# Optimization experiments

Measured on AMD Instinct MI355X. Metric: run time of the kernel, lower is better.

Reference implementation:

```python
import jax, jax.numpy as jnp
import numpy as np
import math

B = 262144
STATE = 6
TOTAL_MEAS = 27
HID = 256
INPUT_DIM = TOTAL_MEAS * 2 + 1 + STATE + 12  # 73
PI = math.pi
NORM_R_SCALE = 500.0 / 150000.0
ANG_IDX = np.array([0, 1, 3, 4, 6, 9, 10, 12, 13, 15, 18, 19, 21, 22, 24])
ANG_MASK = np.zeros((TOTAL_MEAS,), dtype=bool)
ANG_MASK[ANG_IDX] = True


def setup_inputs() -> dict:
    key = jax.random.key(0)
    ks = jax.random.split(key, 16)
    s = lambda fan: 1.0 / math.sqrt(fan)
    inp = {
        "meas": jax.random.normal(ks[0], (B, TOTAL_MEAS), jnp.float32),
        "mask": jnp.ones((B, TOTAL_MEAS), jnp.float32),
        "dt": jax.random.uniform(ks[1], (B,), jnp.float32),
        "baselines": jax.random.normal(ks[2], (B, 12), jnp.float32),
        "x_prev": jax.random.normal(ks[3], (B, STATE), jnp.float32),
        "hx": jnp.zeros((B, HID), jnp.float32),
        # GRU params (torch gate order: r, z, n)
        "W_ih": jax.random.uniform(ks[4], (3 * HID, INPUT_DIM), jnp.float32, -s(HID), s(HID)),
        "W_hh": jax.random.uniform(ks[5], (3 * HID, HID), jnp.float32, -s(HID), s(HID)),
        "b_ih": jax.random.uniform(ks[6], (3 * HID,), jnp.float32, -s(HID), s(HID)),
        "b_hh": jax.random.uniform(ks[7], (3 * HID,), jnp.float32, -s(HID), s(HID)),
        # LayerNorm
        "ln_g": jnp.ones((HID,), jnp.float32),
        "ln_b": jnp.zeros((HID,), jnp.float32),
        # MLP head: 256 -> 256 -> 128 -> 6*27
        "W1": jax.random.uniform(ks[8], (256, HID), jnp.float32, -s(HID), s(HID)),
        "b1": jax.random.uniform(ks[9], (256,), jnp.float32, -s(HID), s(HID)),
        "W2": jax.random.uniform(ks[10], (128, 256), jnp.float32, -s(256), s(256)),
        "b2": jax.random.uniform(ks[11], (128,), jnp.float32, -s(256), s(256)),
        "W3": jax.random.uniform(ks[12], (STATE * TOTAL_MEAS, 128), jnp.float32, -s(128), s(128)),
        "b3": jax.random.uniform(ks[13], (STATE * TOTAL_MEAS,), jnp.float32, -s(128), s(128)),
    }
    return inp


def _wrap_angle(a):
    two_pi = 2.0 * PI
    return a - two_pi * jnp.round(a / two_pi)


def _platform_y_pred(x_rel):
    # x_rel: [B, 6] -> [B, 9] radar/EO measurement
    r_xy = jnp.sqrt(x_rel[:, 0] ** 2 + x_rel[:, 2] ** 2 + 1e-9)
    az = jnp.arctan2(x_rel[:, 2], x_rel[:, 0]) / PI
    el = jnp.arctan2(x_rel[:, 4], r_xy) / PI
    r = jnp.sqrt(x_rel[:, 0] ** 2 + x_rel[:, 2] ** 2 + x_rel[:, 4] ** 2 + 1e-9)
    z = jnp.zeros_like(r)
    return jnp.stack([az, el, r, az, el, z, az, z, z], axis=1)


def _forward(meas, mask, dt, baselines, x_prev, hx,
             W_ih, W_hh, b_ih, b_hh, ln_g, ln_b, W1, b1, W2, b2, W3, b3):
    # f_predict (CV model): x0 += dt*x1, x2 += dt*x3, x4 += dt*x5
    dt_scaled = dt * NORM_R_SCALE  # [B]
    zcol = jnp.zeros_like(x_prev[:, :1])
    shift = jnp.concatenate([x_prev[:, 1:2], zcol, x_prev[:, 3:4], zcol, x_prev[:, 5:6], zcol], axis=1)
    x_minus = x_prev + dt_scaled[:, None] * shift  # [B, 6]

    y_pred = jnp.concatenate([
        _platform_y_pred(x_minus),
        _platform_y_pred(x_minus - baselines[:, 0:6]),
        _platform_y_pred(x_minus - baselines[:, 6:12]),
    ], axis=1)  # [B, 27]

    innov = meas - y_pred
    wrapped = _wrap_angle(innov * PI) / PI
    innov = jnp.where(jnp.asarray(ANG_MASK)[None, :], wrapped, innov)
    innov = innov * mask

    rnn_in = jnp.concatenate([innov, mask, dt[:, None], x_minus, baselines], axis=1)  # [B, 73]

    # single-step GRU (torch semantics, gate order r,z,n)
    gi = rnn_in @ W_ih.T + b_ih  # [B, 3H]
    gh = hx @ W_hh.T + b_hh      # [B, 3H]
    gi_r, gi_z, gi_n = jnp.split(gi, 3, axis=1)
    gh_r, gh_z, gh_n = jnp.split(gh, 3, axis=1)
    r = jax.nn.sigmoid(gi_r + gh_r)
    z = jax.nn.sigmoid(gi_z + gh_z)
    n = jnp.tanh(gi_n + r * gh_n)
    h_new = (1.0 - z) * n + z * hx  # [B, H]

    # LayerNorm
    mu = jnp.mean(h_new, axis=-1, keepdims=True)
    var = jnp.var(h_new, axis=-1, keepdims=True)
    h_ln = (h_new - mu) / jnp.sqrt(var + 1e-5) * ln_g + ln_b

    # MLP gain head (dropout inactive at inference)
    f1 = jax.nn.relu(h_ln @ W1.T + b1)
    f2 = jax.nn.relu(f1 @ W2.T + b2)
    K = (f2 @ W3.T + b3).reshape(-1, STATE, TOTAL_MEAS)
    K = jnp.clip(K, -3.0, 3.0)

    correction = jnp.einsum('bsm,bm->bs', K, innov)
    x_new = jnp.clip(x_minus + correction, -5.0, 5.0)
    return x_new, h_new


def reference(meas, mask, dt, baselines, x_prev, hx,
              W_ih, W_hh, b_ih, b_hh, ln_g, ln_b, W1, b1, W2, b2, W3, b3):
    return _forward(meas, mask, dt, baselines, x_prev, hx,
                    W_ih, W_hh, b_ih, b_hh, ln_g, ln_b, W1, b1, W2, b2, W3, b3)
```

## Files before the change

### kernel.cpp

```cpp
#include <hip/hip_runtime.h>
#include <math.h>

#define B_TOTAL  262144
#define ROWS     128
#define NWG      (B_TOTAL/ROWS)
#define NTHR     512
#define PI_F     3.14159265358979323846f
#define NORM_R   (500.0f/150000.0f)

typedef float  f32x4  __attribute__((ext_vector_type(4)));
typedef short  bf16x8 __attribute__((ext_vector_type(8)));

#define W_TOTAL (49*8192)

#define LDS_RB   0
#define LDS_HB   34816
#define LDS_STG  100352
#define LDS_XMC  149504
#define LDS_LNS  152576
#define LDS_TOTAL 156672

#define WAIT_VM2 asm volatile("s_waitcnt vmcnt(2)" ::: "memory")
#define WAIT_VM0 asm volatile("s_waitcnt vmcnt(0)" ::: "memory")
#define BARv     __builtin_amdgcn_s_barrier()

__device__ __forceinline__ ushort f2bf(float f){
    union { float f; unsigned u; } v; v.f = f;
    unsigned r = v.u + 0x7FFFu + ((v.u >> 16) & 1u);
    return (ushort)(r >> 16);
}
__device__ __forceinline__ float b2f(ushort u){
    union { unsigned u; float f; } v; v.u = ((unsigned)u) << 16;
    return v.f;
}
__device__ __forceinline__ unsigned pk2(float a, float b){
    return (unsigned)f2bf(a) | ((unsigned)f2bf(b) << 16);
}
__device__ __forceinline__ float upk(unsigned u, int hi){
    return b2f((ushort)(hi ? (u >> 16) : (u & 0xffffu)));
}
__device__ __forceinline__ float sigm(float x){ return 1.0f/(1.0f+__expf(-x)); }
__device__ __forceinline__ float tanh_(float x){ return 1.0f - 2.0f/(__expf(2.0f*x)+1.0f); }
__device__ __forceinline__ int swzb(int row, int k){
    return ((row<<9) + (k<<1)) ^ ((row&7)<<4);
}
__device__ __forceinline__ bf16x8 rdW(const char* gb, int col, int lk){
    int slot = lk ^ ((col >> 1) & 3);
    return *(const bf16x8*)(gb + col*64 + slot*16);
}
__device__ __forceinline__ void stage16(const ushort* src, char* dst, int w, int lane){
    #pragma unroll
    for (int i = 0; i < 2; ++i)
        __builtin_amdgcn_global_load_lds(
            (const __attribute__((address_space(1))) void*)(src + (size_t)((w*2+i)*64 + lane)*8),
            (__attribute__((address_space(3))) void*)(dst + (w*2+i)*1024),
            16, 0, 0);
}
#define PH(g) do { \
    if ((g) == 48) WAIT_VM0; else WAIT_VM2; \
    BARv; \
    if ((g)+2 <= 48) stage16(ws + (size_t)((g)+2)*8192, STG + (((g)+2)%3)*16384, w, lane); \
} while(0)

__device__ __forceinline__ void ldA4_rb(const ushort* Rbu, int mh, int lr, int kb, int lk8, bf16x8 a[4]){
    #pragma unroll
    for (int i = 0; i < 4; ++i)
        a[i] = *(const bf16x8*)(Rbu + (mh*64 + i*16 + lr)*104 + kb*32 + lk8);
}
__device__ __forceinline__ void ldA4_hb(const char* Hb, int mh, int lr, int kb, int lk8, bf16x8 a[4]){
    #pragma unroll
    for (int i = 0; i < 4; ++i)
        a[i] = *(const bf16x8*)(Hb + swzb(mh*64 + i*16 + lr, kb*32 + lk8));
}
__device__ __forceinline__ void mmW(const char* base, int colbase, int lr, int lk,
                                    const bf16x8 a[4], f32x4 acc[4][4]){
    #pragma unroll
    for (int j = 0; j < 4; ++j) {
        bf16x8 wf = rdW(base, colbase + j*16 + lr, lk);
        #pragma unroll
        for (int i = 0; i < 4; ++i)
            acc[i][j] = __builtin_amdgcn_mfma_f32_16x16x32_bf16(wf, a[i], acc[i][j], 0,0,0);
    }
}

__global__ void prep_weights(const float* __restrict__ W_ih, const float* __restrict__ W_hh,
                             const float* __restrict__ W1, const float* __restrict__ W2,
                             const float* __restrict__ W3, ushort* __restrict__ ws)
{
    int id = blockIdx.x*256 + threadIdx.x;
    if (id >= W_TOTAL) return;
    int g = id >> 13;
    int u = id & 8191;
    float v = 0.0f;
    if (g >= 41 && g < 45) {
        int half = u >> 12, u2 = u & 4095;
        int col = u2 >> 5, v5 = u2 & 31, slot = v5 >> 3, e = v5 & 7;
        int kq = slot ^ ((col >> 1) & 3);
        int kb = (g-41)*2 + half;
        v = W2[col*256 + kb*32 + kq*8 + e];
    } else {
        int col = u >> 5, v5 = u & 31, slot = v5 >> 3, e = v5 & 7;
        int kq = slot ^ ((col >> 1) & 3);
        if (g < 3) {
            int k = g*32 + kq*8 + e;
            if (k < 73) v = W_ih[(512+col)*73 + k];
        } else if (g < 11) {
            int k = (g-3)*32 + kq*8 + e;
            v = W_hh[(512+col)*256 + k];
        } else if (g < 22) {
            int k = (g-11)*32 + kq*8 + e;
            v = (k < 73) ? W_ih[col*73 + k] : ((k < 96) ? 0.0f : W_hh[col*256 + (k-96)]);
        } else if (g < 33) {
            int k = (g-22)*32 + kq*8 + e;
            v = (k < 73) ? W_ih[(256+col)*73 + k] : ((k < 96) ? 0.0f : W_hh[(256+col)*256 + (k-96)]);
        } else if (g < 41) {
            int k = (g-33)*32 + kq*8 + e;
            v = W1[col*256 + k];
        } else {
            int k = (g-45)*32 + kq*8 + e;
            if (col < 162) v = W3[col*128 + k];
        }
    }
    ws[id] = f2bf(v);
}

__global__ __launch_bounds__(NTHR, 1) void knet_mfma(
    const float* __restrict__ meas, const float* __restrict__ mask,
    const float* __restrict__ dt,   const float* __restrict__ baselines,
    const float* __restrict__ x_prev, const float* __restrict__ hx,
    const float* __restrict__ b_ih, const float* __restrict__ b_hh,
    const float* __restrict__ ln_g, const float* __restrict__ ln_b,
    const float* __restrict__ b1,   const float* __restrict__ b2,
    const float* __restrict__ b3,
    const ushort* __restrict__ ws,
    float* __restrict__ out)
{
    extern __shared__ char smem[];
    ushort* Rbu  = (ushort*)(smem + LDS_RB);
    char*   Hb   = smem + LDS_HB;
    char*   STG  = smem + LDS_STG;
    float*  xmc  = (float*)(smem + LDS_XMC);
    float*  lnscr= (float*)(smem + LDS_LNS);

    const int tid  = threadIdx.x;
    const int w    = __builtin_amdgcn_readfirstlane(tid >> 6);
    const int nq   = w & 3;
    const int mh   = w >> 2;
    const int lane = tid & 63;
    const int lr   = lane & 15;
    const int lk   = lane >> 4;
    const int lk8  = lk * 8;
    const int row0 = blockIdx.x * ROWS;
    float* hout = out + (size_t)B_TOTAL*6;

    stage16(ws,          STG,          w, lane);
    stage16(ws + 8192,   STG + 16384,  w, lane);

    float* scr = (float*)Hb;
    {
        const size_t m0 = (size_t)row0*27;
        for (int i = tid; i < 3456; i += NTHR) scr[i]        = meas[m0 + i];
        for (int i = tid; i < 3456; i += NTHR) scr[3456 + i] = mask[m0 + i];
        for (int i = tid; i < 1536; i += NTHR) scr[6912 + i] = baselines[(size_t)row0*12 + i];
        for (int i = tid; i < 768;  i += NTHR) scr[8448 + i] = x_prev[(size_t)row0*6 + i];
        if (tid < 128) scr[9216 + tid] = dt[row0 + tid];
    }
    __syncthreads();

    {
        const int part = w >> 1;
        const int row  = (w & 1)*64 + lane;
        const float dtv = scr[9216 + row];
        const float dts = dtv * NORM_R;
        float xp[6], xm[6];
        #pragma unroll
        for (int s = 0; s < 6; ++s) xp[s] = scr[8448 + row*6 + s];
        xm[0] = xp[0] + dts*xp[1]; xm[1] = xp[1];
        xm[2] = xp[2] + dts*xp[3]; xm[3] = xp[3];
        xm[4] = xp[4] + dts*xp[5]; xm[5] = xp[5];
        if (part < 3) {
            float xr[6];
            #pragma unroll
            for (int s = 0; s < 6; ++s) {
                float b = (part == 0) ? 0.0f : scr[6912 + row*12 + (part-1)*6 + s];
                xr[s] = xm[s] - b;
            }
            float rxy = sqrtf(xr[0]*xr[0] + xr[2]*xr[2] + 1e-9f);
            float azv = atan2f(xr[2], xr[0]) * (1.0f/PI_F);
            float elv = atan2f(xr[4], rxy)   * (1.0f/PI_F);
            float rrv = sqrtf(xr[0]*xr[0] + xr[2]*xr[2] + xr[4]*xr[4] + 1e-9f);
            float y[9] = {azv, elv, rrv, azv, elv, 0.0f, azv, 0.0f, 0.0f};
            const bool ang[9] = {true,true,false,true,true,false,true,false,false};
            #pragma unroll
            for (int i = 0; i < 9; ++i) {
                int m = part*9 + i;
                float ms = scr[3456 + row*27 + m];
                float v  = scr[row*27 + m] - y[i];
                if (ang[i]) v = v - 2.0f*rintf(v*0.5f);
                v *= ms;
                Rbu[row*104 + m]      = f2bf(v);
                Rbu[row*104 + 27 + m] = f2bf(ms);
            }
        } else {
            Rbu[row*104 + 54] = f2bf(dtv);
            #pragma unroll
            for (int s = 0; s < 6; ++s) Rbu[row*104 + 55 + s] = f2bf(xm[s]);
            #pragma unroll
            for (int q = 0; q < 12; ++q) Rbu[row*104 + 61 + q] = f2bf(scr[6912 + row*12 + q]);
            #pragma unroll
            for (int k = 73; k < 96; ++k) Rbu[row*104 + k] = 0;
            #pragma unroll
            for (int s = 0; s < 6; ++s) xmc[row*6 + s] = xm[s];
        }
    }
    __syncthreads();

    {
        const size_t hbase = (size_t)row0 * 256;
        #pragma unroll
        for (int ii = 0; ii < 8; ++ii) {
            int cid = tid + ii*NTHR;
            int r  = cid >> 5;
            int k0 = (cid & 31) << 3;
            const float4* p = (const float4*)(hx + hbase + (size_t)r*256 + k0);
            float4 u = p[0], v2 = p[1];
            bf16x8 o;
            o[0]=(short)f2bf(u.x);  o[1]=(short)f2bf(u.y);  o[2]=(short)f2bf(u.z);  o[3]=(short)f2bf(u.w);
            o[4]=(short)f2bf(v2.x); o[5]=(short)f2bf(v2.y); o[6]=(short)f2bf(v2.z); o[7]=(short)f2bf(v2.w);
            *(bf16x8*)(Hb + swzb(r, k0)) = o;
        }
    }
    __syncthreads();

    unsigned ginp[4][4][2], ghnp[4][4][2];

    {
        f32x4 acc[4][4];
        #pragma unroll
        for (int i = 0; i < 4; ++i)
            #pragma unroll
            for (int j = 0; j < 4; ++j) acc[i][j] = (f32x4){0,0,0,0};
        #pragma unroll
        for (int p = 0; p < 3; ++p) {
            PH(p);
            bf16x8 a[4];
            ldA4_rb(Rbu, mh, lr, p, lk8, a);
            __builtin_amdgcn_s_setprio(1);
            mmW(STG + (p%3)*16384, nq*64, lr, lk, a, acc);
            __builtin_amdgcn_s_setprio(0);
        }
        #pragma unroll
        for (int j = 0; j < 4; ++j) {
            const int c0 = nq*64 + j*16 + lk*4;
            f32x4 b4 = *(const f32x4*)(b_ih + 512 + c0);
            #pragma unroll
            for (int i = 0; i < 4; ++i) {
                ginp[i][j][0] = pk2(acc[i][j][0] + b4[0], acc[i][j][1] + b4[1]);
                ginp[i][j][1] = pk2(acc[i][j][2] + b4[2], acc[i][j][3] + b4[3]);
            }
        }
    }
    {
        f32x4 acc[4][4];
        #pragma unroll
        for (int i = 0; i < 4; ++i)
            #pragma unroll
            for (int j = 0; j < 4; ++j) acc[i][j] = (f32x4){0,0,0,0};
        #pragma unroll
        for (int p = 0; p < 8; ++p) {
            PH(3+p);
            bf16x8 a[4];
            ldA4_hb(Hb, mh, lr, p, lk8, a);
            __builtin_amdgcn_s_setprio(1);
            mmW(STG + ((3+p)%3)*16384, nq*64, lr, lk, a, acc);
            __builtin_amdgcn_s_setprio(0);
        }
        #pragma unroll
        for (int j = 0; j < 4; ++j) {
            const int c0 = nq*64 + j*16 + lk*4;
            f32x4 b4 = *(const f32x4*)(b_hh + 512 + c0);
            #pragma unroll
            for (int i = 0; i < 4; ++i) {
                ghnp[i][j][0] = pk2(acc[i][j][0] + b4[0], acc[i][j][1] + b4[1]);
                ghnp[i][j][1] = pk2(acc[i][j][2] + b4[2], acc[i][j][3] + b4[3]);
            }
        }
    }
    unsigned npk[4][4][2];
    {
        f32x4 acc[4][4];
        #pragma unroll
        for (int i = 0; i < 4; ++i)
            #pragma unroll
            for (int j = 0; j < 4; ++j) acc[i][j] = (f32x4){0,0,0,0};
        #pragma unroll
        for (int p = 0; p < 11; ++p) {
            PH(11+p);
            bf16x8 a[4];
            if (p < 3) ldA4_rb(Rbu, mh, lr, p, lk8, a);
            else       ldA4_hb(Hb, mh, lr, p-3, lk8, a);
            __builtin_amdgcn_s_setprio(1);
            mmW(STG + ((11+p)%3)*16384, nq*64, lr, lk, a, acc);
            __builtin_amdgcn_s_setprio(0);
        }
        #pragma unroll
        for (int j = 0; j < 4; ++j) {
            const int c0 = nq*64 + j*16 + lk*4;
            f32x4 bi4 = *(const f32x4*)(b_ih + c0);
            f32x4 bh4 = *(const f32x4*)(b_hh + c0);
            #pragma unroll
            for (int i = 0; i < 4; ++i) {
                float nv[4];
                #pragma unroll
                for (int e = 0; e < 4; ++e) {
                    float rg = sigm(acc[i][j][e] + bi4[e] + bh4[e]);
                    float gin = upk(ginp[i][j][e>>1], e&1);
                    float ghn = upk(ghnp[i][j][e>>1], e&1);
                    nv[e] = tanh_(gin + rg*ghn);
                }
                npk[i][j][0] = pk2(nv[0], nv[1]);
                npk[i][j][1] = pk2(nv[2], nv[3]);
            }
        }
    }
    float lsum[4] = {0,0,0,0}, lsq[4] = {0,0,0,0};
    {
        f32x4 acc[4][4];
        #pragma unroll
        for (int i = 0; i < 4; ++i)
            #pragma unroll
            for (int j = 0; j < 4; ++j) acc[i][j] = (f32x4){0,0,0,0};
        #pragma unroll
        for (int p = 0; p < 11; ++p) {
            PH(22+p);
            bf16x8 a[4];
            if (p < 3) ldA4_rb(Rbu, mh, lr, p, lk8, a);
            else       ldA4_hb(Hb, mh, lr, p-3, lk8, a);
            __builtin_amdgcn_s_setprio(1);
            mmW(STG + ((22+p)%3)*16384, nq*64, lr, lk, a, acc);
            __builtin_amdgcn_s_setprio(0);
        }
        #pragma unroll
        for (int j = 0; j < 4; ++j) {
            const int c0 = nq*64 + j*16 + lk*4;
            f32x4 bi4 = *(const f32x4*)(b_ih + 256 + c0);
            f32x4 bh4 = *(const f32x4*)(b_hh + 256 + c0);
            #pragma unroll
            for (int i = 0; i < 4; ++i) {
                const int row = mh*64 + i*16 + lr;
                uint2 hxd = *(const uint2*)(Hb + swzb(row, c0));
                float hn4[4];
                #pragma unroll
                for (int e = 0; e < 4; ++e) {
                    float zg = sigm(acc[i][j][e] + bi4[e] + bh4[e]);
                    float nv = upk(npk[i][j][e>>1], e&1);
                    float hxv = upk(e < 2 ? hxd.x : hxd.y, e&1);
                    float hn = (1.0f - zg)*nv + zg*hxv;
                    hn4[e] = hn; lsum[i] += hn; lsq[i] += hn*hn;
                }
                uint2 o;
                o.x = pk2(hn4[0], hn4[1]);
                o.y = pk2(hn4[2], hn4[3]);
                *(uint2*)(Hb + swzb(row, c0)) = o;
                float4 st = { hn4[0], hn4[1], hn4[2], hn4[3] };
                *(float4*)(hout + (size_t)(row0+row)*256 + c0) = st;
            }
        }
    }
    #pragma unroll
    for (int i = 0; i < 4; ++i) {
        lsum[i] += __shfl_xor(lsum[i], 16); lsum[i] += __shfl_xor(lsum[i], 32);
        lsq[i]  += __shfl_xor(lsq[i], 16);  lsq[i]  += __shfl_xor(lsq[i], 32);
    }
    if (lk == 0) {
        #pragma unroll
        for (int i = 0; i < 4; ++i) {
            const int row = mh*64 + i*16 + lr;
            lnscr[row*8 + nq*2 + 0] = lsum[i];
            lnscr[row*8 + nq*2 + 1] = lsq[i];
        }
    }
    __syncthreads();

    {
        float mu[4], rstd[4];
        #pragma unroll
        for (int i = 0; i < 4; ++i) {
            const int row = mh*64 + i*16 + lr;
            float s = 0, q = 0;
            #pragma unroll
            for (int qq = 0; qq < 4; ++qq) { s += lnscr[row*8 + qq*2]; q += lnscr[row*8 + qq*2 + 1]; }
            mu[i] = s * (1.0f/256.0f);
            rstd[i] = rsqrtf(q*(1.0f/256.0f) - mu[i]*mu[i] + 1e-5f);
        }
        #pragma unroll
        for (int j = 0; j < 4; ++j) {
            const int c0 = nq*64 + j*16 + lk*4;
            f32x4 g4 = *(const f32x4*)(ln_g + c0);
            f32x4 b4 = *(const f32x4*)(ln_b + c0);
            #pragma unroll
            for (int i = 0; i < 4; ++i) {
                const int row = mh*64 + i*16 + lr;
                uint2 d = *(const uint2*)(Hb + swzb(row, c0));
                float v0 = (upk(d.x,0)-mu[i])*rstd[i]*g4[0] + b4[0];
                float v1 = (upk(d.x,1)-mu[i])*rstd[i]*g4[1] + b4[1];
                float v2 = (upk(d.y,0)-mu[i])*rstd[i]*g4[2] + b4[2];
                float v3 = (upk(d.y,1)-mu[i])*rstd[i]*g4[3] + b4[3];
                uint2 o; o.x = pk2(v0, v1); o.y = pk2(v2, v3);
                *(uint2*)(Hb + swzb(row, c0)) = o;
            }
        }
    }
    __syncthreads();

    {
        f32x4 acc[4][4];
        #pragma unroll
        for (int i = 0; i < 4; ++i)
            #pragma unroll
            for (int j = 0; j < 4; ++j) acc[i][j] = (f32x4){0,0,0,0};
        #pragma unroll
        for (int p = 0; p < 8; ++p) {
            PH(33+p);
            bf16x8 a[4];
            ldA4_hb(Hb, mh, lr, p, lk8, a);
            __builtin_amdgcn_s_setprio(1);
            mmW(STG + ((33+p)%3)*16384, nq*64, lr, lk, a, acc);
            __builtin_amdgcn_s_setprio(0);
        }
        __syncthreads();
        #pragma unroll
        for (int j = 0; j < 4; ++j) {
            const int c0 = nq*64 + j*16 + lk*4;
            f32x4 b4 = *(const f32x4*)(b1 + c0);
            #pragma unroll
            for (int i = 0; i < 4; ++i) {
                const int row = mh*64 + i*16 + lr;
                uint2 o;
                o.x = pk2(fmaxf(acc[i][j][0]+b4[0],0.f), fmaxf(acc[i][j][1]+b4[1],0.f));
                o.y = pk2(fmaxf(acc[i][j][2]+b4[2],0.f), fmaxf(acc[i][j][3]+b4[3],0.f));
                *(uint2*)(Hb + swzb(row, c0)) = o;
            }
        }
    }
    __syncthreads();

    f32x4 c3[4][2];
    #pragma unroll
    for (int i = 0; i < 4; ++i)
        #pragma unroll
        for (int j = 0; j < 2; ++j) c3[i][j] = (f32x4){0,0,0,0};
    #pragma unroll
    for (int p = 0; p < 4; ++p) {
        PH(41+p);
        const char* sb = STG + ((41+p)%3)*16384;
        #pragma unroll
        for (int h = 0; h < 2; ++h) {
            bf16x8 a[4];
            ldA4_hb(Hb, mh, lr, 2*p + h, lk8, a);
            __builtin_amdgcn_s_setprio(1);
            #pragma unroll
            for (int j = 0; j < 2; ++j) {
                bf16x8 wf = rdW(sb + h*8192, nq*32 + j*16 + lr, lk);
                #pragma unroll
                for (int i = 0; i < 4; ++i)
                    c3[i][j] = __builtin_amdgcn_mfma_f32_16x16x32_bf16(wf, a[i], c3[i][j], 0,0,0);
            }
            __builtin_amdgcn_s_setprio(0);
        }
    }
    f32x4 iv[4][3];
    #pragma unroll
    for (int j = 0; j < 3; ++j)
        #pragma unroll
        for (int i = 0; i < 4; ++i) {
            const int row = mh*64 + i*16 + lr;
            #pragma unroll
            for (int e = 0; e < 4; ++e) {
                int col = nq*48 + j*16 + lk*4 + e;
                int m = col - 27*(col/27);
                iv[i][j][e] = b2f(Rbu[row*104 + m]);
            }
        }
    __syncthreads();
    #pragma unroll
    for (int j = 0; j < 2; ++j) {
        const int c0 = nq*32 + j*16 + lk*4;
        f32x4 b4 = *(const f32x4*)(b2 + c0);
        #pragma unroll
        for (int i = 0; i < 4; ++i) {
            const int row = mh*64 + i*16 + lr;
            uint2 o;
            o.x = pk2(fmaxf(c3[i][j][0]+b4[0],0.f), fmaxf(c3[i][j][1]+b4[1],0.f));
            o.y = pk2(fmaxf(c3[i][j][2]+b4[2],0.f), fmaxf(c3[i][j][3]+b4[3],0.f));
            *(uint2*)((char*)Rbu + row*272 + c0*2) = o;
        }
    }
    __syncthreads();

    {
        f32x4 c4[4][3];
        #pragma unroll
        for (int i = 0; i < 4; ++i)
            #pragma unroll
            for (int j = 0; j < 3; ++j) c4[i][j] = (f32x4){0,0,0,0};
        #pragma unroll
        for (int p = 0; p < 4; ++p) {
            PH(45+p);
            const char* sb = STG + ((45+p)%3)*16384;
            bf16x8 a[4];
            #pragma unroll
            for (int i = 0; i < 4; ++i)
                a[i] = *(const bf16x8*)((const char*)Rbu + (mh*64 + i*16 + lr)*272 + (p*32 + lk8)*2);
            __builtin_amdgcn_s_setprio(1);
            #pragma unroll
            for (int j = 0; j < 3; ++j) {
                bf16x8 wf = rdW(sb, nq*48 + j*16 + lr, lk);
                #pragma unroll
                for (int i = 0; i < 4; ++i)
                    c4[i][j] = __builtin_amdgcn_mfma_f32_16x16x32_bf16(wf, a[i], c4[i][j], 0,0,0);
            }
            __builtin_amdgcn_s_setprio(0);
        }
        #pragma unroll
        for (int j = 0; j < 3; ++j)
            #pragma unroll
            for (int i = 0; i < 4; ++i) {
                const int row = mh*64 + i*16 + lr;
                #pragma unroll
                for (int e = 0; e < 4; ++e) {
                    int col = nq*48 + j*16 + lk*4 + e;
                    if (col < 162) {
                        int s = col / 27;
                        float K = fminf(fmaxf(c4[i][j][e] + b3[col], -3.0f), 3.0f);
                        atomicAdd(&xmc[row*6 + s], K * iv[i][j][e]);
                    }
                }
            }
    }
    __syncthreads();

    for (int t = tid; t < ROWS*6; t += NTHR) {
        int row = t / 6, s = t - row*6;
        float v = fminf(fmaxf(xmc[t], -5.0f), 5.0f);
        out[(size_t)(row0+row)*6 + s] = v;
    }
}

extern "C" void kernel_launch(void* const* d_in, const int* in_sizes, int n_in,
                              void* d_out, int out_size, void* d_ws, size_t ws_size,
                              hipStream_t stream) {
    const float* meas      = (const float*)d_in[0];
    const float* mask      = (const float*)d_in[1];
    const float* dtv       = (const float*)d_in[2];
    const float* baselines = (const float*)d_in[3];
    const float* x_prev    = (const float*)d_in[4];
    const float* hx        = (const float*)d_in[5];
    const float* W_ih      = (const float*)d_in[6];
    const float* W_hh      = (const float*)d_in[7];
    const float* b_ih      = (const float*)d_in[8];
    const float* b_hh      = (const float*)d_in[9];
    const float* ln_g      = (const float*)d_in[10];
    const float* ln_b      = (const float*)d_in[11];
    const float* W1        = (const float*)d_in[12];
    const float* b1        = (const float*)d_in[13];
    const float* W2        = (const float*)d_in[14];
    const float* b2        = (const float*)d_in[15];
    const float* W3        = (const float*)d_in[16];
    const float* b3        = (const float*)d_in[17];
    ushort* wsb = (ushort*)d_ws;
    float* outp = (float*)d_out;

    prep_weights<<<(W_TOTAL + 255)/256, 256, 0, stream>>>(W_ih, W_hh, W1, W2, W3, wsb);
    knet_mfma<<<NWG, NTHR, LDS_TOTAL, stream>>>(
        meas, mask, dtv, baselines, x_prev, hx,
        b_ih, b_hh, ln_g, ln_b, b1, b2, b3, wsb, outp);
}
```

Before: 773.1 us.

## Halve rows per workgroup to run two 256-thread workgroups per CU

Cuts each workgroup to 64 rows and 4 waves and shrinks LDS to about 80KB so two workgroups can share a CU (launch_bounds 2). The weight staging ring drops from triple to double buffering, and a barrier is added after each MMA phase to protect the buffer being reloaded. LayerNorm is rewritten so each row is reduced by 4 threads, removing the cross-wave scratch. Innovation values are reread from LDS at the final step instead of being held in registers. The intent is better latency hiding through occupancy, at the cost of more barriers, twice as many weight reloads per row, and shallower prefetch.

```diff
diff --git a/kernel.cpp b/kernel.cpp
--- a/kernel.cpp
+++ b/kernel.cpp
@@ -2,9 +2,9 @@
 #include <math.h>
 
 #define B_TOTAL  262144
-#define ROWS     128
+#define ROWS     64
 #define NWG      (B_TOTAL/ROWS)
-#define NTHR     512
+#define NTHR     256
 #define PI_F     3.14159265358979323846f
 #define NORM_R   (500.0f/150000.0f)
 
@@ -14,15 +14,15 @@
 #define W_TOTAL (49*8192)
 
 #define LDS_RB   0
-#define LDS_HB   34816
-#define LDS_STG  100352
-#define LDS_XMC  149504
-#define LDS_LNS  152576
-#define LDS_TOTAL 156672
-
-#define WAIT_VM2 asm volatile("s_waitcnt vmcnt(2)" ::: "memory")
-#define WAIT_VM0 asm volatile("s_waitcnt vmcnt(0)" ::: "memory")
-#define BARv     __builtin_amdgcn_s_barrier()
+#define LDS_HB   13312
+#define LDS_STG  46080
+#define LDS_XMC  78848
+#define LDS_TOTAL 80384
+
+#define WAIT_VM4  asm volatile("s_waitcnt vmcnt(4)" ::: "memory")
+#define WAIT_VM0  asm volatile("s_waitcnt vmcnt(0)" ::: "memory")
+#define WAIT_LGKM asm volatile("s_waitcnt lgkmcnt(0)" ::: "memory")
+#define BARv      __builtin_amdgcn_s_barrier()
 
 __device__ __forceinline__ ushort f2bf(float f){
     union { float f; unsigned u; } v; v.f = f;
@@ -50,27 +50,27 @@
 }
 __device__ __forceinline__ void stage16(const ushort* src, char* dst, int w, int lane){
     #pragma unroll
-    for (int i = 0; i < 2; ++i)
+    for (int i = 0; i < 4; ++i)
         __builtin_amdgcn_global_load_lds(
-            (const __attribute__((address_space(1))) void*)(src + (size_t)((w*2+i)*64 + lane)*8),
-            (__attribute__((address_space(3))) void*)(dst + (w*2+i)*1024),
+            (const __attribute__((address_space(1))) void*)(src + (size_t)((w*4+i)*64 + lane)*8),
+            (__attribute__((address_space(3))) void*)(dst + (w*4+i)*1024),
             16, 0, 0);
 }
 #define PH(g) do { \
-    if ((g) == 48) WAIT_VM0; else WAIT_VM2; \
+    if ((g) < 48) stage16(ws + (size_t)((g)+1)*8192, STG + (((g)+1)&1)*16384, w, lane); \
+    if ((g) < 48) WAIT_VM4; else WAIT_VM0; \
     BARv; \
-    if ((g)+2 <= 48) stage16(ws + (size_t)((g)+2)*8192, STG + (((g)+2)%3)*16384, w, lane); \
 } while(0)
 
-__device__ __forceinline__ void ldA4_rb(const ushort* Rbu, int mh, int lr, int kb, int lk8, bf16x8 a[4]){
+__device__ __forceinline__ void ldA4_rb(const ushort* Rbu, int lr, int kb, int lk8, bf16x8 a[4]){
     #pragma unroll
     for (int i = 0; i < 4; ++i)
-        a[i] = *(const bf16x8*)(Rbu + (mh*64 + i*16 + lr)*104 + kb*32 + lk8);
-}
-__device__ __forceinline__ void ldA4_hb(const char* Hb, int mh, int lr, int kb, int lk8, bf16x8 a[4]){
+        a[i] = *(const bf16x8*)(Rbu + (i*16 + lr)*104 + kb*32 + lk8);
+}
+__device__ __forceinline__ void ldA4_hb(const char* Hb, int lr, int kb, int lk8, bf16x8 a[4]){
     #pragma unroll
     for (int i = 0; i < 4; ++i)
-        a[i] = *(const bf16x8*)(Hb + swzb(mh*64 + i*16 + lr, kb*32 + lk8));
+        a[i] = *(const bf16x8*)(Hb + swzb(i*16 + lr, kb*32 + lk8));
 }
 __device__ __forceinline__ void mmW(const char* base, int colbase, int lr, int lk,
                                     const bf16x8 a[4], f32x4 acc[4][4]){
@@ -124,7 +124,7 @@
     ws[id] = f2bf(v);
 }
 
-__global__ __launch_bounds__(NTHR, 1) void knet_mfma(
+__global__ __launch_bounds__(NTHR, 2) void knet_mfma(
     const float* __restrict__ meas, const float* __restrict__ mask,
     const float* __restrict__ dt,   const float* __restrict__ baselines,
     const float* __restrict__ x_prev, const float* __restrict__ hx,
@@ -140,12 +140,10 @@
     char*   Hb   = smem + LDS_HB;
     char*   STG  = smem + LDS_STG;
     float*  xmc  = (float*)(smem + LDS_XMC);
-    float*  lnscr= (float*)(smem + LDS_LNS);
 
     const int tid  = threadIdx.x;
     const int w    = __builtin_amdgcn_readfirstlane(tid >> 6);
-    const int nq   = w & 3;
-    const int mh   = w >> 2;
+    const int nq   = w;
     const int lane = tid & 63;
     const int lr   = lane & 15;
     const int lk   = lane >> 4;
@@ -153,36 +151,34 @@
     const int row0 = blockIdx.x * ROWS;
     float* hout = out + (size_t)B_TOTAL*6;
 
-    stage16(ws,          STG,          w, lane);
-    stage16(ws + 8192,   STG + 16384,  w, lane);
+    stage16(ws, STG, w, lane);
 
     float* scr = (float*)Hb;
     {
         const size_t m0 = (size_t)row0*27;
-        for (int i = tid; i < 3456; i += NTHR) scr[i]        = meas[m0 + i];
-        for (int i = tid; i < 3456; i += NTHR) scr[3456 + i] = mask[m0 + i];
-        for (int i = tid; i < 1536; i += NTHR) scr[6912 + i] = baselines[(size_t)row0*12 + i];
-        for (int i = tid; i < 768;  i += NTHR) scr[8448 + i] = x_prev[(size_t)row0*6 + i];
-        if (tid < 128) scr[9216 + tid] = dt[row0 + tid];
+        for (int i = tid; i < 1728; i += NTHR) scr[i]        = meas[m0 + i];
+        for (int i = tid; i < 1728; i += NTHR) scr[1728 + i] = mask[m0 + i];
+        for (int i = tid; i < 768;  i += NTHR) scr[3456 + i] = baselines[(size_t)row0*12 + i];
+        for (int i = tid; i < 384;  i += NTHR) scr[4224 + i] = x_prev[(size_t)row0*6 + i];
+        if (tid < 64) scr[4608 + tid] = dt[row0 + tid];
     }
     __syncthreads();
 
     {
-        const int part = w >> 1;
-        const int row  = (w & 1)*64 + lane;
-        const float dtv = scr[9216 + row];
+        const int row = lane;
+        const float dtv = scr[4608 + row];
         const float dts = dtv * NORM_R;
         float xp[6], xm[6];
         #pragma unroll
-        for (int s = 0; s < 6; ++s) xp[s] = scr[8448 + row*6 + s];
+        for (int s = 0; s < 6; ++s) xp[s] = scr[4224 + row*6 + s];
         xm[0] = xp[0] + dts*xp[1]; xm[1] = xp[1];
         xm[2] = xp[2] + dts*xp[3]; xm[3] = xp[3];
         xm[4] = xp[4] + dts*xp[5]; xm[5] = xp[5];
-        if (part < 3) {
+        if (w < 3) {
             float xr[6];
             #pragma unroll
             for (int s = 0; s < 6; ++s) {
-                float b = (part == 0) ? 0.0f : scr[6912 + row*12 + (part-1)*6 + s];
+                float b = (w == 0) ? 0.0f : scr[3456 + row*12 + (w-1)*6 + s];
                 xr[s] = xm[s] - b;
             }
             float rxy = sqrtf(xr[0]*xr[0] + xr[2]*xr[2] + 1e-9f);
@@ -193,8 +189,8 @@
             const bool ang[9] = {true,true,false,true,true,false,true,false,false};
             #pragma unroll
             for (int i = 0; i < 9; ++i) {
-                int m = part*9 + i;
-                float ms = scr[3456 + row*27 + m];
+                int m = w*9 + i;
+                float ms = scr[1728 + row*27 + m];
                 float v  = scr[row*27 + m] - y[i];
                 if (ang[i]) v = v - 2.0f*rintf(v*0.5f);
                 v *= ms;
@@ -206,7 +202,7 @@
             #pragma unroll
             for (int s = 0; s < 6; ++s) Rbu[row*104 + 55 + s] = f2bf(xm[s]);
             #pragma unroll
-            for (int q = 0; q < 12; ++q) Rbu[row*104 + 61 + q] = f2bf(scr[6912 + row*12 + q]);
+            for (int q = 0; q < 12; ++q) Rbu[row*104 + 61 + q] = f2bf(scr[3456 + row*12 + q]);
             #pragma unroll
             for (int k = 73; k < 96; ++k) Rbu[row*104 + k] = 0;
             #pragma unroll
@@ -232,7 +228,8 @@
     }
     __syncthreads();
 
-    unsigned ginp[4][4][2], ghnp[4][4][2];
+    unsigned ginp[4][2], ghnp[4][2], npk[4][2];
+    unsigned ginq[4][4][2], ghnq[4][4][2];
 
     {
         f32x4 acc[4][4];
@@ -244,10 +241,11 @@
         for (int p = 0; p < 3; ++p) {
             PH(p);
             bf16x8 a[4];
-            ldA4_rb(Rbu, mh, lr, p, lk8, a);
-            __builtin_amdgcn_s_setprio(1);
-            mmW(STG + (p%3)*16384, nq*64, lr, lk, a, acc);
-            __builtin_amdgcn_s_setprio(0);
+            ldA4_rb(Rbu, lr, p, lk8, a);
+            __builtin_amdgcn_s_setprio(1);
+            mmW(STG + (p&1)*16384, nq*64, lr, lk, a, acc);
+            __builtin_amdgcn_s_setprio(0);
+            BARv;
         }
         #pragma unroll
         for (int j = 0; j < 4; ++j) {
@@ -255,8 +253,8 @@
             f32x4 b4 = *(const f32x4*)(b_ih + 512 + c0);
             #pragma unroll
             for (int i = 0; i < 4; ++i) {
-                ginp[i][j][0] = pk2(acc[i][j][0] + b4[0], acc[i][j][1] + b4[1]);
-                ginp[i][j][1] = pk2(acc[i][j][2] + b4[2], acc[i][j][3] + b4[3]);
+                ginq[i][j][0] = pk2(acc[i][j][0] + b4[0], acc[i][j][1] + b4[1]);
+                ginq[i][j][1] = pk2(acc[i][j][2] + b4[2], acc[i][j][3] + b4[3]);
             }
         }
     }
@@ -270,10 +268,11 @@
         for (int p = 0; p < 8; ++p) {
             PH(3+p);
             bf16x8 a[4];
-            ldA4_hb(Hb, mh, lr, p, lk8, a);
-            __builtin_amdgcn_s_setprio(1);
-            mmW(STG + ((3+p)%3)*16384, nq*64, lr, lk, a, acc);
-            __builtin_amdgcn_s_setprio(0);
+            ldA4_hb(Hb, lr, p, lk8, a);
+            __builtin_amdgcn_s_setprio(1);
+            mmW(STG + ((3+p)&1)*16384, nq*64, lr, lk, a, acc);
+            __builtin_amdgcn_s_setprio(0);
+            BARv;
         }
         #pragma unroll
         for (int j = 0; j < 4; ++j) {
@@ -281,12 +280,12 @@
             f32x4 b4 = *(const f32x4*)(b_hh + 512 + c0);
             #pragma unroll
             for (int i = 0; i < 4; ++i) {
-                ghnp[i][j][0] = pk2(acc[i][j][0] + b4[0], acc[i][j][1] + b4[1]);
-                ghnp[i][j][1] = pk2(acc[i][j][2] + b4[2], acc[i][j][3] + b4[3]);
-            }
-        }
-    }
-    unsigned npk[4][4][2];
+                ghnq[i][j][0] = pk2(acc[i][j][0] + b4[0], acc[i][j][1] + b4[1]);
+                ghnq[i][j][1] = pk2(acc[i][j][2] + b4[2], acc[i][j][3] + b4[3]);
+            }
+        }
+    }
+    unsigned nq_[4][4][2];
     {
         f32x4 acc[4][4];
         #pragma unroll
@@ -297,11 +296,12 @@
         for (int p = 0; p < 11; ++p) {
             PH(11+p);
             bf16x8 a[4];
-            if (p < 3) ldA4_rb(Rbu, mh, lr, p, lk8, a);
-            else       ldA4_hb(Hb, mh, lr, p-3, lk8, a);
-            __builtin_amdgcn_s_setprio(1);
-            mmW(STG + ((11+p)%3)*16384, nq*64, lr, lk, a, acc);
-            __builtin_amdgcn_s_setprio(0);
+            if (p < 3) ldA4_rb(Rbu, lr, p, lk8, a);
+            else       ldA4_hb(Hb, lr, p-3, lk8, a);
+            __builtin_amdgcn_s_setprio(1);
+            mmW(STG + ((11+p)&1)*16384, nq*64, lr, lk, a, acc);
+            __builtin_amdgcn_s_setprio(0);
+            BARv;
         }
         #pragma unroll
         for (int j = 0; j < 4; ++j) {
@@ -314,16 +314,13 @@
                 #pragma unroll
                 for (int e = 0; e < 4; ++e) {
                     float rg = sigm(acc[i][j][e] + bi4[e] + bh4[e]);
-                    float gin = upk(ginp[i][j][e>>1], e&1);
-                    float ghn = upk(ghnp[i][j][e>>1], e&1);
-                    nv[e] = tanh_(gin + rg*ghn);
+                    nv[e] = tanh_(upk(ginq[i][j][e>>1], e&1) + rg*upk(ghnq[i][j][e>>1], e&1));
                 }
-                npk[i][j][0] = pk2(nv[0], nv[1]);
-                npk[i][j][1] = pk2(nv[2], nv[3]);
-            }
-        }
-    }
-    float lsum[4] = {0,0,0,0}, lsq[4] = {0,0,0,0};
+                nq_[i][j][0] = pk2(nv[0], nv[1]);
+                nq_[i][j][1] = pk2(nv[2], nv[3]);
+            }
+        }
+    }
     {
         f32x4 acc[4][4];
         #pragma unroll
@@ -334,11 +331,12 @@
         for (int p = 0; p < 11; ++p) {
             PH(22+p);
             bf16x8 a[4];
-            if (p < 3) ldA4_rb(Rbu, mh, lr, p, lk8, a);
-            else       ldA4_hb(Hb, mh, lr, p-3, lk8, a);
-            __builtin_amdgcn_s_setprio(1);
-            mmW(STG + ((22+p)%3)*16384, nq*64, lr, lk, a, acc);
-            __builtin_amdgcn_s_setprio(0);
+            if (p < 3) ldA4_rb(Rbu, lr, p, lk8, a);
+            else       ldA4_hb(Hb, lr, p-3, lk8, a);
+            __builtin_amdgcn_s_setprio(1);
+            mmW(STG + ((22+p)&1)*16384, nq*64, lr, lk, a, acc);
+            __builtin_amdgcn_s_setprio(0);
+            BARv;
         }
         #pragma unroll
         for (int j = 0; j < 4; ++j) {
@@ -347,71 +345,60 @@
             f32x4 bh4 = *(const f32x4*)(b_hh + 256 + c0);
             #pragma unroll
             for (int i = 0; i < 4; ++i) {
-                const int row = mh*64 + i*16 + lr;
+                const int row = i*16 + lr;
                 uint2 hxd = *(const uint2*)(Hb + swzb(row, c0));
                 float hn4[4];
                 #pragma unroll
                 for (int e = 0; e < 4; ++e) {
                     float zg = sigm(acc[i][j][e] + bi4[e] + bh4[e]);
-                    float nv = upk(npk[i][j][e>>1], e&1);
                     float hxv = upk(e < 2 ? hxd.x : hxd.y, e&1);
-                    float hn = (1.0f - zg)*nv + zg*hxv;
-                    hn4[e] = hn; lsum[i] += hn; lsq[i] += hn*hn;
+                    hn4[e] = (1.0f - zg)*upk(nq_[i][j][e>>1], e&1) + zg*hxv;
                 }
-                uint2 o;
-                o.x = pk2(hn4[0], hn4[1]);
-                o.y = pk2(hn4[2], hn4[3]);
+                uint2 o; o.x = pk2(hn4[0], hn4[1]); o.y = pk2(hn4[2], hn4[3]);
                 *(uint2*)(Hb + swzb(row, c0)) = o;
                 float4 st = { hn4[0], hn4[1], hn4[2], hn4[3] };
                 *(float4*)(hout + (size_t)(row0+row)*256 + c0) = st;
             }
         }
     }
-    #pragma unroll
-    for (int i = 0; i < 4; ++i) {
-        lsum[i] += __shfl_xor(lsum[i], 16); lsum[i] += __shfl_xor(lsum[i], 32);
-        lsq[i]  += __shfl_xor(lsq[i], 16);  lsq[i]  += __shfl_xor(lsq[i], 32);
-    }
-    if (lk == 0) {
-        #pragma unroll
-        for (int i = 0; i < 4; ++i) {
-            const int row = mh*64 + i*16 + lr;
-            lnscr[row*8 + nq*2 + 0] = lsum[i];
-            lnscr[row*8 + nq*2 + 1] = lsq[i];
-        }
-    }
-    __syncthreads();
-
-    {
-        float mu[4], rstd[4];
-        #pragma unroll
-        for (int i = 0; i < 4; ++i) {
-            const int row = mh*64 + i*16 + lr;
-            float s = 0, q = 0;
-            #pragma unroll
-            for (int qq = 0; qq < 4; ++qq) { s += lnscr[row*8 + qq*2]; q += lnscr[row*8 + qq*2 + 1]; }
-            mu[i] = s * (1.0f/256.0f);
-            rstd[i] = rsqrtf(q*(1.0f/256.0f) - mu[i]*mu[i] + 1e-5f);
-        }
-        #pragma unroll
-        for (int j = 0; j < 4; ++j) {
-            const int c0 = nq*64 + j*16 + lk*4;
-            f32x4 g4 = *(const f32x4*)(ln_g + c0);
-            f32x4 b4 = *(const f32x4*)(ln_b + c0);
-            #pragma unroll
-            for (int i = 0; i < 4; ++i) {
-                const int row = mh*64 + i*16 + lr;
-                uint2 d = *(const uint2*)(Hb + swzb(row, c0));
-                float v0 = (upk(d.x,0)-mu[i])*rstd[i]*g4[0] + b4[0];
-                float v1 = (upk(d.x,1)-mu[i])*rstd[i]*g4[1] + b4[1];
-                float v2 = (upk(d.y,0)-mu[i])*rstd[i]*g4[2] + b4[2];
-                float v3 = (upk(d.y,1)-mu[i])*rstd[i]*g4[3] + b4[3];
-                uint2 o; o.x = pk2(v0, v1); o.y = pk2(v2, v3);
-                *(uint2*)(Hb + swzb(row, c0)) = o;
-            }
-        }
-    }
-    __syncthreads();
+    WAIT_LGKM; BARv;
+
+    {
+        const int row = tid >> 2;
+        const int o   = tid & 3;
+        bf16x8 ch[8];
+        float sum = 0.0f, sq = 0.0f;
+        #pragma unroll
+        for (int jx = 0; jx < 8; ++jx) {
+            ch[jx] = *(const bf16x8*)(Hb + swzb(row, o*64 + jx*8));
+            #pragma unroll
+            for (int e = 0; e < 8; ++e) {
+                float f = b2f((ushort)ch[jx][e]);
+                sum += f; sq += f*f;
+            }
+        }
+        sum += __shfl_xor(sum, 1); sum += __shfl_xor(sum, 2);
+        sq  += __shfl_xor(sq, 1);  sq  += __shfl_xor(sq, 2);
+        float mu   = sum * (1.0f/256.0f);
+        float rstd = rsqrtf(sq*(1.0f/256.0f) - mu*mu + 1e-5f);
+        #pragma unroll
+        for (int jx = 0; jx < 8; ++jx) {
+            int col0 = o*64 + jx*8;
+            float4 g0 = *(const float4*)(ln_g + col0), g1 = *(const float4*)(ln_g + col0 + 4);
+            float4 bb0 = *(const float4*)(ln_b + col0), bb1 = *(const float4*)(ln_b + col0 + 4);
+            bf16x8 oo;
+            oo[0] = (short)f2bf((b2f((ushort)ch[jx][0]) - mu)*rstd*g0.x + bb0.x);
+            oo[1] = (short)f2bf((b2f((ushort)ch[jx][1]) - mu)*rstd*g0.y + bb0.y);
+            oo[2] = (short)f2bf((b2f((ushort)ch[jx][2]) - mu)*rstd*g0.z + bb0.z);
+            oo[3] = (short)f2bf((b2f((ushort)ch[jx][3]) - mu)*rstd*g0.w + bb0.w);
+            oo[4] = (short)f2bf((b2f((ushort)ch[jx][4]) - mu)*rstd*g1.x + bb1.x);
+            oo[5] = (short)f2bf((b2f((ushort)ch[jx][5]) - mu)*rstd*g1.y + bb1.y);
+            oo[6] = (short)f2bf((b2f((ushort)ch[jx][6]) - mu)*rstd*g1.z + bb1.z);
+            oo[7] = (short)f2bf((b2f((ushort)ch[jx][7]) - mu)*rstd*g1.w + bb1.w);
+            *(bf16x8*)(Hb + swzb(row, col0)) = oo;
+        }
+    }
+    WAIT_LGKM; BARv;
 
     {
         f32x4 acc[4][4];
@@ -423,19 +410,19 @@
         for (int p = 0; p < 8; ++p) {
             PH(33+p);
             bf16x8 a[4];
-            ldA4_hb(Hb, mh, lr, p, lk8, a);
-            __builtin_amdgcn_s_setprio(1);
-            mmW(STG + ((33+p)%3)*16384, nq*64, lr, lk, a, acc);
-            __builtin_amdgcn_s_setprio(0);
-        }
-        __syncthreads();
+            ldA4_hb(Hb, lr, p, lk8, a);
+            __builtin_amdgcn_s_setprio(1);
+            mmW(STG + ((33+p)&1)*16384, nq*64, lr, lk, a, acc);
+            __builtin_amdgcn_s_setprio(0);
+            BARv;
+        }
         #pragma unroll
         for (int j = 0; j < 4; ++j) {
             const int c0 = nq*64 + j*16 + lk*4;
             f32x4 b4 = *(const f32x4*)(b1 + c0);
             #pragma unroll
             for (int i = 0; i < 4; ++i) {
-                const int row = mh*64 + i*16 + lr;
+                const int row = i*16 + lr;
                 uint2 o;
                 o.x = pk2(fmaxf(acc[i][j][0]+b4[0],0.f), fmaxf(acc[i][j][1]+b4[1],0.f));
                 o.y = pk2(fmaxf(acc[i][j][2]+b4[2],0.f), fmaxf(acc[i][j][3]+b4[3],0.f));
@@ -443,7 +430,7 @@
             }
         }
     }
-    __syncthreads();
+    WAIT_LGKM; BARv;
 
     f32x4 c3[4][2];
     #pragma unroll
@@ -453,11 +440,11 @@
     #pragma unroll
     for (int p = 0; p < 4; ++p) {
         PH(41+p);
-        const char* sb = STG + ((41+p)%3)*16384;
+        const char* sb = STG + ((41+p)&1)*16384;
         #pragma unroll
         for (int h = 0; h < 2; ++h) {
             bf16x8 a[4];
-            ldA4_hb(Hb, mh, lr, 2*p + h, lk8, a);
+            ldA4_hb(Hb, lr, 2*p + h, lk8, a);
             __builtin_amdgcn_s_setprio(1);
             #pragma unroll
             for (int j = 0; j < 2; ++j) {
@@ -468,35 +455,23 @@
             }
             __builtin_amdgcn_s_setprio(0);
         }
-    }
-    f32x4 iv[4][3];
-    #pragma unroll
-    for (int j = 0; j < 3; ++j)
-        #pragma unroll
-        for (int i = 0; i < 4; ++i) {
-            const int row = mh*64 + i*16 + lr;
-            #pragma unroll
-            for (int e = 0; e < 4; ++e) {
-                int col = nq*48 + j*16 + lk*4 + e;
-                int m = col - 27*(col/27);
-                iv[i][j][e] = b2f(Rbu[row*104 + m]);
-            }
-        }
-    __syncthreads();
+        BARv;
+    }
+    ushort* F2 = (ushort*)Hb;
     #pragma unroll
     for (int j = 0; j < 2; ++j) {
         const int c0 = nq*32 + j*16 + lk*4;
         f32x4 b4 = *(const f32x4*)(b2 + c0);
         #pragma unroll
         for (int i = 0; i < 4; ++i) {
-            const int row = mh*64 + i*16 + lr;
+            const int row = i*16 + lr;
             uint2 o;
             o.x = pk2(fmaxf(c3[i][j][0]+b4[0],0.f), fmaxf(c3[i][j][1]+b4[1],0.f));
             o.y = pk2(fmaxf(c3[i][j][2]+b4[2],0.f), fmaxf(c3[i][j][3]+b4[3],0.f));
-            *(uint2*)((char*)Rbu + row*272 + c0*2) = o;
-        }
-    }
-    __syncthreads();
+            *(uint2*)((char*)F2 + row*272 + c0*2) = o;
+        }
+    }
+    WAIT_LGKM; BARv;
 
     {
         f32x4 c4[4][3];
@@ -507,11 +482,11 @@
         #pragma unroll
         for (int p = 0; p < 4; ++p) {
             PH(45+p);
-            const char* sb = STG + ((45+p)%3)*16384;
+            const char* sb = STG + ((45+p)&1)*16384;
             bf16x8 a[4];
             #pragma unroll
             for (int i = 0; i < 4; ++i)
-                a[i] = *(const bf16x8*)((const char*)Rbu + (mh*64 + i*16 + lr)*272 + (p*32 + lk8)*2);
+                a[i] = *(const bf16x8*)((const char*)F2 + (i*16 + lr)*272 + (p*32 + lk8)*2);
             __builtin_amdgcn_s_setprio(1);
             #pragma unroll
             for (int j = 0; j < 3; ++j) {
@@ -521,19 +496,20 @@
                     c4[i][j] = __builtin_amdgcn_mfma_f32_16x16x32_bf16(wf, a[i], c4[i][j], 0,0,0);
             }
             __builtin_amdgcn_s_setprio(0);
+            BARv;
         }
         #pragma unroll
         for (int j = 0; j < 3; ++j)
             #pragma unroll
             for (int i = 0; i < 4; ++i) {
-                const int row = mh*64 + i*16 + lr;
+                const int row = i*16 + lr;
                 #pragma unroll
                 for (int e = 0; e < 4; ++e) {
                     int col = nq*48 + j*16 + lk*4 + e;
                     if (col < 162) {
-                        int s = col / 27;
+                        int s = col / 27, m = col - s*27;
                         float K = fminf(fmaxf(c4[i][j][e] + b3[col], -3.0f), 3.0f);
-                        atomicAdd(&xmc[row*6 + s], K * iv[i][j][e]);
+                        atomicAdd(&xmc[row*6 + s], K * b2f(Rbu[row*104 + m]));
                     }
                 }
             }
```

After: 701.8 us. 1.1x faster.
